# Performance work log

Hardware: AMD Instinct MI355X
Metric: run time of the kernel (lower is better)

## Reference

```python
import jax, jax.numpy as jnp
import numpy as np

B, T, E, M, V = 256, 256, 512, 16, 32000
EPS = 1e-6


def layer_norm(x, g, b):
    m = x.mean(-1, keepdims=True)
    v = x.var(-1, keepdims=True)
    return (x - m) / jnp.sqrt(v + EPS) * g + b


def setup_inputs() -> dict:
    key = jax.random.key(0)
    ks = jax.random.split(key, 12)
    s = 0.02
    return {
        "hidden_state": jax.random.normal(ks[0], (B, 1, E), jnp.float32),
        "output_sequence": jax.random.randint(ks[1], (B, T), 0, V),
        "emb_out": jax.random.normal(ks[2], (V, E), jnp.float32) * s,
        "Wq": jax.random.normal(ks[3], (E, E), jnp.float32) * s,
        "bq": jnp.zeros((E,), jnp.float32),
        "Wk": jax.random.normal(ks[4], (E, E), jnp.float32) * s,
        "bk": jnp.zeros((E,), jnp.float32),
        "Wv": jax.random.normal(ks[5], (E, E), jnp.float32) * s,
        "bv": jnp.zeros((E,), jnp.float32),
        "mover_w": jax.random.normal(ks[6], (M, E), jnp.float32) * s,  # decoder_mover.weight
        "gamma": jnp.ones((E,), jnp.float32),
        "beta": jnp.zeros((E,), jnp.float32),
        "vocab_W": jax.random.normal(ks[7], (E, V), jnp.float32) * s,
        "vocab_b": jnp.zeros((V,), jnp.float32),
    }


def reference(hidden_state, output_sequence, emb_out, Wq, bq, Wk, bk, Wv, bv,
              mover_w, gamma, beta, vocab_W, vocab_b):
    # Embeddings: lookup * sqrt(embed_dim) (annotated-transformer convention)
    x = emb_out[output_sequence] * jnp.sqrt(jnp.float32(E))  # [B, T, E]
    b = x.shape[0]
    # mover = (zeros_like(z)+1) * weight[None]  -> broadcast weight over batch
    mover = jnp.broadcast_to(mover_w[None], (b, M, E))
    # Precompute K/V projections of the constant mover rows once per step inside scan
    scale = 1.0 / jnp.sqrt(jnp.float32(E))

    def step(z, xt):                       # z: [B, E], xt: [B, E]
        z = z + xt
        g = jnp.concatenate([z[:, None, :], mover], axis=1)  # [B, 1+M, E]
        # only row 0 of dg is used -> query only the z token (same math)
        q = z @ Wq + bq                    # [B, E]
        k = g @ Wk + bk                    # [B, 1+M, E]
        v = g @ Wv + bv                    # [B, 1+M, E]
        att = jax.nn.softmax(jnp.einsum('be,bne->bn', q, k) * scale, axis=-1)
        dg0 = jnp.einsum('bn,bne->be', att, v)
        z = layer_norm(z + dg0, gamma, beta)
        return z, None

    z0 = hidden_state[:, 0, :]
    z, _ = jax.lax.scan(step, z0, jnp.swapaxes(x, 0, 1))
    z = z[:, None, :]                      # [B, 1, E]
    y = jax.nn.log_softmax(z @ vocab_W + vocab_b, axis=-1)  # [B, 1, V]
    return (z, y)
```

## Files before the change

### kernel.cpp

```cpp
#include <hip/hip_runtime.h>

#define B_ 256
#define T_ 256
#define E_ 512
#define V_ 32000
#define NMOV 16
#define NT 65
#define NCG 16
#define NBG 16
#define YSTR 1056
#define ZSTR 520

#define SQRTE 22.62741699796952f
#define SCALE 0.04419417382415922f

typedef __attribute__((ext_vector_type(8))) short bf16x8;
typedef __attribute__((ext_vector_type(4))) short bf16x4;
typedef __attribute__((ext_vector_type(4))) float f32x4;
typedef unsigned long long u64;

__device__ __forceinline__ short f2bf(float f) {
  unsigned u = __float_as_uint(f);
  u += 0x7fffu + ((u >> 16) & 1u);
  return (short)(u >> 16);
}
__device__ __forceinline__ float bf2f(short s) {
  return __uint_as_float(((unsigned)(unsigned short)s) << 16);
}

__device__ __forceinline__ float wredsum(float v) {
  int x;
  x = __builtin_amdgcn_update_dpp(0, __float_as_int(v), 0xB1, 0xF, 0xF, true);
  v += __int_as_float(x);
  x = __builtin_amdgcn_update_dpp(0, __float_as_int(v), 0x4E, 0xF, 0xF, true);
  v += __int_as_float(x);
  x = __builtin_amdgcn_update_dpp(0, __float_as_int(v), 0x141, 0xF, 0xF, true);
  v += __int_as_float(x);
  x = __builtin_amdgcn_update_dpp(0, __float_as_int(v), 0x140, 0xF, 0xF, true);
  v += __int_as_float(x);
  x = __builtin_amdgcn_update_dpp(0, __float_as_int(v), 0x142, 0xF, 0xF, true);
  v += __int_as_float(x);
  x = __builtin_amdgcn_update_dpp(0, __float_as_int(v), 0x143, 0xF, 0xF, true);
  v += __int_as_float(x);
  return __int_as_float(__builtin_amdgcn_readlane(__float_as_int(v), 63));
}

__device__ __forceinline__ bf16x8 aload8v(const short* p) {
  union { u64 u[2]; bf16x8 v; } c;
  c.u[0] = __hip_atomic_load((const u64*)p,       __ATOMIC_RELAXED, __HIP_MEMORY_SCOPE_AGENT);
  c.u[1] = __hip_atomic_load((const u64*)(p + 4), __ATOMIC_RELAXED, __HIP_MEMORY_SCOPE_AGENT);
  return c.v;
}
__device__ __forceinline__ void astore4v(short* p, bf16x4 v) {
  union { bf16x4 v; u64 u; } c; c.v = v;
  __hip_atomic_store((u64*)p, c.u, __ATOMIC_RELAXED, __HIP_MEMORY_SCOPE_AGENT);
}

__global__ void k_movers(const float* __restrict__ Wk, const float* __restrict__ bk,
                         const float* __restrict__ Wv, const float* __restrict__ bv,
                         const float* __restrict__ mover, float* __restrict__ kmvm)
{
  const int m = blockIdx.x & 15;
  const int s = blockIdx.x >> 4;
  const float* W  = s ? Wv : Wk;
  const float* bb = s ? bv : bk;
  const int c = threadIdx.x * 2;
  float a0 = bb[c], a1 = bb[c + 1];
  for (int r = 0; r < E_; ++r) {
    float mv = mover[m * E_ + r];
    float2 wv = *(const float2*)(W + (size_t)r * E_ + c);
    a0 += mv * wv.x; a1 += mv * wv.y;
  }
  kmvm[(s * NMOV + m) * E_ + c]     = a0;
  kmvm[(s * NMOV + m) * E_ + c + 1] = a1;
}

__global__ void k_gemmA(const float* __restrict__ Wq, const float* __restrict__ Wk,
                        float* __restrict__ A)
{
  const int ti = blockIdx.x >> 5, tj = blockIdx.x & 31;
  const int l = threadIdx.x, r16 = l & 15, kq = (l >> 4) * 8;
  f32x4 acc = {0.f, 0.f, 0.f, 0.f};
  for (int ks = 0; ks < 16; ++ks) {
    const float* ap = Wq + (size_t)(ti * 16 + r16) * E_ + ks * 32 + kq;
    const float* bp = Wk + (size_t)(tj * 16 + r16) * E_ + ks * 32 + kq;
    bf16x8 a, b;
    #pragma unroll
    for (int j = 0; j < 8; ++j) { a[j] = f2bf(ap[j]); b[j] = f2bf(bp[j]); }
    acc = __builtin_amdgcn_mfma_f32_16x16x32_bf16(a, b, acc, 0, 0, 0);
  }
  #pragma unroll
  for (int r = 0; r < 4; ++r)
    A[(size_t)(ti * 16 + (l >> 4) * 4 + r) * E_ + tj * 16 + r16] = acc[r];
}

__global__ void k_wqk(const float* __restrict__ Wq, const float* __restrict__ kmvm,
                      float* __restrict__ Wqk)
{
  const int i = blockIdx.x;
  const int l = threadIdx.x, m = l & 15, sl = l >> 4;
  float p = 0.f;
  for (int j = sl * 128; j < sl * 128 + 128; ++j)
    p += Wq[(size_t)i * E_ + j] * kmvm[(size_t)m * E_ + j];
  p += __shfl_xor(p, 16, 64);
  p += __shfl_xor(p, 32, 64);
  if (l < 16) Wqk[i * 16 + m] = p;
}

__global__ void k_cvec(const float* __restrict__ Wq, const float* __restrict__ Wk,
                       const float* __restrict__ bq, const float* __restrict__ bk,
                       float* __restrict__ cvec)
{
  const int i = blockIdx.x * 64 + threadIdx.x;
  float s = 0.f;
  for (int j = 0; j < E_; ++j)
    s += Wq[(size_t)i * E_ + j] * bk[j] + Wk[(size_t)i * E_ + j] * bq[j];
  cvec[i] = s;
}

__global__ void k_lb(const float* __restrict__ bq, const float* __restrict__ bk,
                     const float* __restrict__ kmvm, float* __restrict__ lb)
{
  const int l = threadIdx.x;
  if (l < 16) {
    float s = 0.f;
    for (int j = 0; j < E_; ++j) s += bq[j] * kmvm[(size_t)l * E_ + j];
    lb[l] = s;
  } else if (l == 16) {
    float s = 0.f;
    for (int j = 0; j < E_; ++j) s += bq[j] * bk[j];
    lb[16] = s;
  }
}

__global__ void k_pack(const float* __restrict__ A, const float* __restrict__ Wv,
                       const float* __restrict__ Wqk, short* __restrict__ Wfrag)
{
  const int blk = blockIdx.x;
  const int ct = blk >> 4, ks = blk & 15;
  const int l = threadIdx.x;
  const int c = ct * 16 + (l & 15);
  const int r0 = ks * 32 + (l >> 4) * 8;
  short v[8];
  #pragma unroll
  for (int j = 0; j < 8; ++j) {
    const int r = r0 + j;
    float x;
    if (c < 512)       x = A[(size_t)r * E_ + c];
    else if (c < 1024) x = Wv[(size_t)r * E_ + (c - 512)];
    else               x = Wqk[r * 16 + (c - 1024)];
    v[j] = f2bf(x);
  }
  *(bf16x8*)(Wfrag + ((size_t)blk * 64 + l) * 8) = *(const bf16x8*)v;
}

__global__ __launch_bounds__(512, 2) void k_scan5(
    const float* __restrict__ hidden, const int* __restrict__ seq,
    const float* __restrict__ emb,
    const float* __restrict__ gamma, const float* __restrict__ beta,
    const float* __restrict__ bv,
    const float* __restrict__ kmvm, const float* __restrict__ cvec,
    const float* __restrict__ lb, const short* __restrict__ Wfrag,
    short* __restrict__ Yx, unsigned* __restrict__ flags,
    float* __restrict__ zout)
{
  extern __shared__ char smem[];
  short* wlds = (short*)smem;
  short* zfs  = (short*)(smem + 81920);
  short* vml  = (short*)(smem + 98304);
  float* cl   = (float*)(smem + 114688);
  float* bvl  = (float*)(smem + 116736);
  float* gl   = (float*)(smem + 118784);
  float* bl   = (float*)(smem + 120832);
  float* lbl  = (float*)(smem + 122880);

  const int tid = threadIdx.x, l = tid & 63, w = tid >> 6;
  const int cg = blockIdx.x >> 4;
  const int bg = blockIdx.x & 15;
  const int ntiles = (cg == 15) ? 5 : 4;

  for (int i = tid; i < NMOV * E_; i += 512)
    vml[i] = f2bf(kmvm[NMOV * E_ + i]);
  for (int i = tid; i < E_; i += 512) {
    cl[i] = cvec[i]; bvl[i] = bv[i]; gl[i] = gamma[i]; bl[i] = beta[i];
  }
  if (tid < 17) lbl[tid] = lb[tid];
  {
    const bf16x8* src = (const bf16x8*)(Wfrag + (size_t)(cg * 4) * 16 * 64 * 8);
    bf16x8* dst = (bf16x8*)wlds;
    for (int i = tid; i < ntiles * 16 * 64; i += 512) dst[i] = src[i];
  }

  const int b0 = bg * 16 + w * 2;
  float zr[2][8];
  #pragma unroll
  for (int bi = 0; bi < 2; ++bi) {
    *(float4*)&zr[bi][0] = *(const float4*)(hidden + (size_t)(b0 + bi) * E_ + l * 8);
    *(float4*)&zr[bi][4] = *(const float4*)(hidden + (size_t)(b0 + bi) * E_ + l * 8 + 4);
  }

  const int sq0 = b0 * T_, sq1 = (b0 + 1) * T_;
  int ian = seq[sq0], ibn = seq[sq1];
  float4 ea0 = *(const float4*)(emb + (size_t)ian * E_ + l * 8);
  float4 ea1 = *(const float4*)(emb + (size_t)ian * E_ + l * 8 + 4);
  float4 eb0 = *(const float4*)(emb + (size_t)ibn * E_ + l * 8);
  float4 eb1 = *(const float4*)(emb + (size_t)ibn * E_ + l * 8 + 4);
  ian = seq[sq0 + 1]; ibn = seq[sq1 + 1];

  unsigned* const flagline = flags + bg * 32;
  __syncthreads();

  #pragma unroll 1
  for (int t = 0; t < T_; ++t) {
    const int p = t & 1;
    {
      float xa[8] = {ea0.x, ea0.y, ea0.z, ea0.w, ea1.x, ea1.y, ea1.z, ea1.w};
      float xb[8] = {eb0.x, eb0.y, eb0.z, eb0.w, eb1.x, eb1.y, eb1.z, eb1.w};
      short ta[8], tb[8];
      #pragma unroll
      for (int j = 0; j < 8; ++j) {
        zr[0][j] += xa[j] * SQRTE; ta[j] = f2bf(zr[0][j]);
        zr[1][j] += xb[j] * SQRTE; tb[j] = f2bf(zr[1][j]);
      }
      const int ks = l >> 2;
      const int ua = ((l & 3) << 4) | (w * 2);
      const int ub = ua | 1;
      *(bf16x8*)&zfs[((ks << 6) + (ua ^ (ks & 7))) * 8] = *(const bf16x8*)ta;
      *(bf16x8*)&zfs[((ks << 6) + (ub ^ (ks & 7))) * 8] = *(const bf16x8*)tb;
    }
    if (t + 1 < T_) {
      ea0 = *(const float4*)(emb + (size_t)ian * E_ + l * 8);
      ea1 = *(const float4*)(emb + (size_t)ian * E_ + l * 8 + 4);
      eb0 = *(const float4*)(emb + (size_t)ibn * E_ + l * 8);
      eb1 = *(const float4*)(emb + (size_t)ibn * E_ + l * 8 + 4);
      if (t + 2 < T_) { ian = seq[sq0 + t + 2]; ibn = seq[sq1 + t + 2]; }
    }
    __syncthreads();

    if (w < ntiles) {
      const int lt = w;
      f32x4 acc = {0.f, 0.f, 0.f, 0.f};
      #pragma unroll
      for (int ks = 0; ks < 16; ++ks) {
        bf16x8 wf = *(const bf16x8*)&wlds[((lt * 16 + ks) * 64 + l) * 8];
        bf16x8 zb = *(const bf16x8*)&zfs[((ks << 6) + (l ^ (ks & 7))) * 8];
        acc = __builtin_amdgcn_mfma_f32_16x16x32_bf16(wf, zb, acc, 0, 0, 0);
      }
      const int gt = cg * 4 + lt;
      bf16x4 o;
      #pragma unroll
      for (int r = 0; r < 4; ++r) o[r] = f2bf(acc[r]);
      astore4v(Yx + (((size_t)(p * NBG + bg) * 16) + (l & 15)) * YSTR
                  + gt * 16 + ((l >> 4) << 2), o);
      asm volatile("s_waitcnt vmcnt(0)" ::: "memory");
    }
    __syncthreads();

    if (tid == 0)
      __hip_atomic_store(&flagline[cg], (unsigned)(t + 1),
                         __ATOMIC_RELAXED, __HIP_MEMORY_SCOPE_AGENT);
    if (w == 0) {
      const unsigned rnd = (unsigned)(t + 1);
      const unsigned* fp = flagline + (l & 15);
      while (__hip_atomic_load(fp, __ATOMIC_RELAXED, __HIP_MEMORY_SCOPE_AGENT) < rnd)
        __builtin_amdgcn_s_sleep(1);
      asm volatile("" ::: "memory");
    }
    __syncthreads();

    {
      const short* Yb  = Yx + ((size_t)(p * NBG + bg) * 16) * YSTR;
      const short* Yr0 = Yb + (size_t)(w * 2) * YSTR;
      const short* Yr1 = Yb + (size_t)(w * 2 + 1) * YSTR;
      bf16x8 wv0 = aload8v(Yr0 + l * 8),       wv1 = aload8v(Yr1 + l * 8);
      bf16x8 vv0 = aload8v(Yr0 + 512 + l * 8), vv1 = aload8v(Yr1 + 512 + l * 8);
      bf16x8 ma0 = aload8v(Yr0 + 1024),        ma1 = aload8v(Yr1 + 1024);
      bf16x8 mb0 = aload8v(Yr0 + 1032),        mb1 = aload8v(Yr1 + 1032);

      float cw[8];
      *(float4*)&cw[0] = *(const float4*)&cl[l * 8];
      *(float4*)&cw[4] = *(const float4*)&cl[l * 8 + 4];
      float p0 = 0.f, p1 = 0.f;
      #pragma unroll
      for (int j = 0; j < 8; ++j) {
        p0 += (bf2f(wv0[j]) + cw[j]) * zr[0][j];
        p1 += (bf2f(wv1[j]) + cw[j]) * zr[1][j];
      }
      const float r0 = wredsum(p0);
      const float r1 = wredsum(p1);

      float a0[17], a1[17];
      a0[0] = (r0 + lbl[16]) * SCALE;
      a1[0] = (r1 + lbl[16]) * SCALE;
      #pragma unroll
      for (int m = 0; m < 8; ++m) {
        a0[m + 1] = (bf2f(ma0[m]) + lbl[m]) * SCALE;
        a0[m + 9] = (bf2f(mb0[m]) + lbl[m + 8]) * SCALE;
        a1[m + 1] = (bf2f(ma1[m]) + lbl[m]) * SCALE;
        a1[m + 9] = (bf2f(mb1[m]) + lbl[m + 8]) * SCALE;
      }
      float mx0 = a0[0], mx1 = a1[0];
      #pragma unroll
      for (int n = 1; n < 17; ++n) { mx0 = fmaxf(mx0, a0[n]); mx1 = fmaxf(mx1, a1[n]); }
      float d0 = 0.f, d1 = 0.f;
      #pragma unroll
      for (int n = 0; n < 17; ++n) {
        a0[n] = __expf(a0[n] - mx0); d0 += a0[n];
        a1[n] = __expf(a1[n] - mx1); d1 += a1[n];
      }
      const float rd0 = __fdividef(1.f, d0);
      const float rd1 = __fdividef(1.f, d1);

      float bw[8];
      *(float4*)&bw[0] = *(const float4*)&bvl[l * 8];
      *(float4*)&bw[4] = *(const float4*)&bvl[l * 8 + 4];
      float u0[8], u1[8];
      #pragma unroll
      for (int j = 0; j < 8; ++j) {
        u0[j] = a0[0] * (bf2f(vv0[j]) + bw[j]);
        u1[j] = a1[0] * (bf2f(vv1[j]) + bw[j]);
      }
      #pragma unroll
      for (int m = 0; m < 16; ++m) {
        const bf16x8 vm = *(const bf16x8*)&vml[m * E_ + l * 8];
        #pragma unroll
        for (int j = 0; j < 8; ++j) {
          const float f = bf2f(vm[j]);
          u0[j] += a0[m + 1] * f;
          u1[j] += a1[m + 1] * f;
        }
      }
      #pragma unroll
      for (int j = 0; j < 8; ++j) {
        u0[j] = zr[0][j] + u0[j] * rd0;
        u1[j] = zr[1][j] + u1[j] * rd1;
      }

      float s10 = 0.f, s20 = 0.f, s11 = 0.f, s21 = 0.f;
      #pragma unroll
      for (int j = 0; j < 8; ++j) {
        s10 += u0[j]; s20 += u0[j] * u0[j];
        s11 += u1[j]; s21 += u1[j] * u1[j];
      }
      s10 = wredsum(s10); s20 = wredsum(s20);
      s11 = wredsum(s11); s21 = wredsum(s21);
      const float mean0 = s10 * (1.f / 512.f);
      const float mean1 = s11 * (1.f / 512.f);
      const float rstd0 = rsqrtf(s20 * (1.f / 512.f) - mean0 * mean0 + 1e-6f);
      const float rstd1 = rsqrtf(s21 * (1.f / 512.f) - mean1 * mean1 + 1e-6f);

      float gw[8], bb[8];
      *(float4*)&gw[0] = *(const float4*)&gl[l * 8];
      *(float4*)&gw[4] = *(const float4*)&gl[l * 8 + 4];
      *(float4*)&bb[0] = *(const float4*)&bl[l * 8];
      *(float4*)&bb[4] = *(const float4*)&bl[l * 8 + 4];
      #pragma unroll
      for (int j = 0; j < 8; ++j) {
        zr[0][j] = (u0[j] - mean0) * rstd0 * gw[j] + bb[j];
        zr[1][j] = (u1[j] - mean1) * rstd1 * gw[j] + bb[j];
      }
    }
  }

  if (cg == 0) {
    #pragma unroll
    for (int bi = 0; bi < 2; ++bi) {
      *(float4*)(zout + (size_t)(b0 + bi) * E_ + l * 8)     = *(float4*)&zr[bi][0];
      *(float4*)(zout + (size_t)(b0 + bi) * E_ + l * 8 + 4) = *(float4*)&zr[bi][4];
    }
  }
}

#define K2_SMEM (128 * ZSTR * 2)

__global__ __launch_bounds__(512, 2) void k_logits(
    const float* __restrict__ z, const float* __restrict__ W,
    const float* __restrict__ bia, float* __restrict__ out)
{
  extern __shared__ short zl[];
  const int tid = threadIdx.x;
  const int btile = blockIdx.x & 1;
  const int vt = blockIdx.x >> 1;
  for (int i = tid; i < 128 * 128; i += 512) {
    int row = i >> 7, c4 = (i & 127) << 2;
    float4 zv = *(const float4*)(z + (size_t)(btile * 128 + row) * E_ + c4);
    short* d = zl + row * ZSTR + c4;
    d[0] = f2bf(zv.x); d[1] = f2bf(zv.y); d[2] = f2bf(zv.z); d[3] = f2bf(zv.w);
  }
  __syncthreads();
  const int lane = tid & 63, w = tid >> 6;
  const int vc = vt * 128 + w * 16 + (lane & 15);
  const int kq = (lane >> 4) * 8;
  f32x4 acc[8];
  #pragma unroll
  for (int rt = 0; rt < 8; ++rt) acc[rt] = (f32x4){0.f, 0.f, 0.f, 0.f};
  for (int ks = 0; ks < 16; ++ks) {
    bf16x8 bf;
    #pragma unroll
    for (int j = 0; j < 8; ++j)
      bf[j] = f2bf(W[(size_t)(ks * 32 + kq + j) * V_ + vc]);
    #pragma unroll
    for (int rt = 0; rt < 8; ++rt) {
      bf16x8 a = *(const bf16x8*)&zl[(rt * 16 + (lane & 15)) * ZSTR + ks * 32 + kq];
      acc[rt] = __builtin_amdgcn_mfma_f32_16x16x32_bf16(a, bf, acc[rt], 0, 0, 0);
    }
  }
  const float bbv = bia[vc];
  #pragma unroll
  for (int rt = 0; rt < 8; ++rt)
    #pragma unroll
    for (int r = 0; r < 4; ++r)
      out[(size_t)(btile * 128 + rt * 16 + (lane >> 4) * 4 + r) * V_ + vc] = acc[rt][r] + bbv;
}

__global__ void k_logsoftmax(float* __restrict__ y)
{
  float* L = y + (size_t)blockIdx.x * V_;
  float m = -3.402823466e+38f, s = 0.f;
  for (int i = threadIdx.x; i < V_; i += 256) {
    float l = L[i];
    if (l > m) { s = s * __expf(m - l) + 1.f; m = l; }
    else       { s += __expf(l - m); }
  }
  #pragma unroll
  for (int k = 1; k < 64; k <<= 1) {
    float m2 = __shfl_xor(m, k, 64);
    float s2 = __shfl_xor(s, k, 64);
    float M = fmaxf(m, m2);
    s = s * __expf(m - M) + s2 * __expf(m2 - M);
    m = M;
  }
  __shared__ float ms[4], ss[4];
  if ((threadIdx.x & 63) == 0) { ms[threadIdx.x >> 6] = m; ss[threadIdx.x >> 6] = s; }
  __syncthreads();
  float M = fmaxf(fmaxf(ms[0], ms[1]), fmaxf(ms[2], ms[3]));
  float S = ss[0] * __expf(ms[0] - M) + ss[1] * __expf(ms[1] - M) +
            ss[2] * __expf(ms[2] - M) + ss[3] * __expf(ms[3] - M);
  const float lse = M + logf(S);
  for (int i = threadIdx.x; i < V_; i += 256) L[i] -= lse;
}

#define SCAN_SMEM 123008

extern "C" void kernel_launch(void* const* d_in, const int* in_sizes, int n_in,
                              void* d_out, int out_size, void* d_ws, size_t ws_size,
                              hipStream_t stream) {
  const float* hidden = (const float*)d_in[0];
  const int*   seq    = (const int*)  d_in[1];
  const float* emb    = (const float*)d_in[2];
  const float* Wq     = (const float*)d_in[3];
  const float* bq     = (const float*)d_in[4];
  const float* Wk     = (const float*)d_in[5];
  const float* bk     = (const float*)d_in[6];
  const float* Wv     = (const float*)d_in[7];
  const float* bv     = (const float*)d_in[8];
  const float* mover  = (const float*)d_in[9];
  const float* gamma  = (const float*)d_in[10];
  const float* beta   = (const float*)d_in[11];
  const float* vocabW = (const float*)d_in[12];
  const float* vocabB = (const float*)d_in[13];

  float* zoutp = (float*)d_out;
  float* yout  = zoutp + (size_t)B_ * E_;

  short*    Wfrag = (short*)yout;
  float*    A     = yout + 266240;
  float*    Wqk   = A + 262144;
  float*    cvec  = Wqk + 8192;
  float*    lbp   = cvec + 512;
  float*    kmvmS = lbp + 32;
  short*    Yx    = (short*)(kmvmS + 16384);
  unsigned* flags = (unsigned*)(Yx + 540672);

  hipMemsetAsync(flags, 0, 16 * 32 * 4, stream);
  hipLaunchKernelGGL(k_movers, dim3(32), dim3(256), 0, stream, Wk, bk, Wv, bv, mover, kmvmS);
  hipLaunchKernelGGL(k_gemmA,  dim3(1024), dim3(64), 0, stream, Wq, Wk, A);
  hipLaunchKernelGGL(k_wqk,    dim3(512), dim3(64), 0, stream, Wq, kmvmS, Wqk);
  hipLaunchKernelGGL(k_cvec,   dim3(8), dim3(64), 0, stream, Wq, Wk, bq, bk, cvec);
  hipLaunchKernelGGL(k_lb,     dim3(1), dim3(64), 0, stream, bq, bk, kmvmS, lbp);
  hipLaunchKernelGGL(k_pack,   dim3(NT * 16), dim3(64), 0, stream, A, Wv, Wqk, Wfrag);

  hipFuncSetAttribute((const void*)k_scan5, hipFuncAttributeMaxDynamicSharedMemorySize, SCAN_SMEM);
  void* args[] = {(void*)&hidden, (void*)&seq, (void*)&emb,
                  (void*)&gamma, (void*)&beta, (void*)&bv,
                  (void*)&kmvmS, (void*)&cvec, (void*)&lbp, (void*)&Wfrag,
                  (void*)&Yx, (void*)&flags, (void*)&zoutp};
  hipLaunchCooperativeKernel((const void*)k_scan5, dim3(NCG * NBG), dim3(512),
                             args, SCAN_SMEM, stream);

  hipFuncSetAttribute((const void*)k_logits, hipFuncAttributeMaxDynamicSharedMemorySize, K2_SMEM);
  hipLaunchKernelGGL(k_logits, dim3(500), dim3(512), K2_SMEM, stream, zoutp, vocabW, vocabB, yout);
  hipLaunchKernelGGL(k_logsoftmax, dim3(256), dim3(256), 0, stream, yout);
}
```

Baseline: 1.521 ms.

## Compute mover attention-weighted sum with MFMA and wave-parallel softmax

```diff
diff --git a/kernel.cpp b/kernel.cpp
--- a/kernel.cpp
+++ b/kernel.cpp
@@ -43,6 +43,33 @@
   x = __builtin_amdgcn_update_dpp(0, __float_as_int(v), 0x143, 0xF, 0xF, true);
   v += __int_as_float(x);
   return __int_as_float(__builtin_amdgcn_readlane(__float_as_int(v), 63));
+}
+__device__ __forceinline__ float rowmax16(float v) {
+  int x;
+  x = __builtin_amdgcn_update_dpp(0, __float_as_int(v), 0xB1, 0xF, 0xF, true);
+  v = fmaxf(v, __int_as_float(x));
+  x = __builtin_amdgcn_update_dpp(0, __float_as_int(v), 0x4E, 0xF, 0xF, true);
+  v = fmaxf(v, __int_as_float(x));
+  x = __builtin_amdgcn_update_dpp(0, __float_as_int(v), 0x141, 0xF, 0xF, true);
+  v = fmaxf(v, __int_as_float(x));
+  x = __builtin_amdgcn_update_dpp(0, __float_as_int(v), 0x140, 0xF, 0xF, true);
+  v = fmaxf(v, __int_as_float(x));
+  return v;
+}
+__device__ __forceinline__ float rowsum16(float v) {
+  int x;
+  x = __builtin_amdgcn_update_dpp(0, __float_as_int(v), 0xB1, 0xF, 0xF, true);
+  v += __int_as_float(x);
+  x = __builtin_amdgcn_update_dpp(0, __float_as_int(v), 0x4E, 0xF, 0xF, true);
+  v += __int_as_float(x);
+  x = __builtin_amdgcn_update_dpp(0, __float_as_int(v), 0x141, 0xF, 0xF, true);
+  v += __int_as_float(x);
+  x = __builtin_amdgcn_update_dpp(0, __float_as_int(v), 0x140, 0xF, 0xF, true);
+  v += __int_as_float(x);
+  return v;
+}
+__device__ __forceinline__ float rdlane(float v, int lane) {
+  return __int_as_float(__builtin_amdgcn_readlane(__float_as_int(v), lane));
 }
 
 __device__ __forceinline__ bf16x8 aload8v(const short* p) {
@@ -154,7 +181,7 @@
   *(bf16x8*)(Wfrag + ((size_t)blk * 64 + l) * 8) = *(const bf16x8*)v;
 }
 
-__global__ __launch_bounds__(512, 2) void k_scan5(
+__global__ __launch_bounds__(512, 2) void k_scan6(
     const float* __restrict__ hidden, const int* __restrict__ seq,
     const float* __restrict__ emb,
     const float* __restrict__ gamma, const float* __restrict__ beta,
@@ -165,31 +192,45 @@
     float* __restrict__ zout)
 {
   extern __shared__ char smem[];
-  short* wlds = (short*)smem;
-  short* zfs  = (short*)(smem + 81920);
-  short* vml  = (short*)(smem + 98304);
-  float* cl   = (float*)(smem + 114688);
-  float* bvl  = (float*)(smem + 116736);
-  float* gl   = (float*)(smem + 118784);
-  float* bl   = (float*)(smem + 120832);
-  float* lbl  = (float*)(smem + 122880);
+  short* wlds    = (short*)smem;
+  short* zfs     = (short*)(smem + 81920);
+  short* vmfragT = (short*)(smem + 98304);
+  float* umov    = (float*)(smem + 114688);
+  short* attf    = (short*)(smem + 147968);
 
   const int tid = threadIdx.x, l = tid & 63, w = tid >> 6;
   const int cg = blockIdx.x >> 4;
   const int bg = blockIdx.x & 15;
   const int ntiles = (cg == 15) ? 5 : 4;
-
-  for (int i = tid; i < NMOV * E_; i += 512)
-    vml[i] = f2bf(kmvm[NMOV * E_ + i]);
-  for (int i = tid; i < E_; i += 512) {
-    cl[i] = cvec[i]; bvl[i] = bv[i]; gl[i] = gamma[i]; bl[i] = beta[i];
-  }
-  if (tid < 17) lbl[tid] = lb[tid];
+  const int lm = l & 15;
+
+  for (int i = tid; i < 32 * 32; i += 512) {
+    const int tile = i >> 5, ln = i & 31;
+    const int m0 = (ln >> 4) * 8, c = tile * 16 + (ln & 15);
+    short tmp[8];
+    #pragma unroll
+    for (int j = 0; j < 8; ++j)
+      tmp[j] = f2bf(kmvm[NMOV * E_ + (size_t)(m0 + j) * E_ + c]);
+    *(bf16x8*)&vmfragT[((size_t)tile * 32 + ln) * 8] = *(const bf16x8*)tmp;
+  }
+  for (int i = tid; i < 16 * 40; i += 512) attf[i] = 0;
   {
     const bf16x8* src = (const bf16x8*)(Wfrag + (size_t)(cg * 4) * 16 * 64 * 8);
     bf16x8* dst = (bf16x8*)wlds;
     for (int i = tid; i < ntiles * 16 * 64; i += 512) dst[i] = src[i];
   }
+
+  float cw[8], bw[8], gw[8], bb[8];
+  *(float4*)&cw[0] = *(const float4*)(cvec  + l * 8);
+  *(float4*)&cw[4] = *(const float4*)(cvec  + l * 8 + 4);
+  *(float4*)&bw[0] = *(const float4*)(bv    + l * 8);
+  *(float4*)&bw[4] = *(const float4*)(bv    + l * 8 + 4);
+  *(float4*)&gw[0] = *(const float4*)(gamma + l * 8);
+  *(float4*)&gw[4] = *(const float4*)(gamma + l * 8 + 4);
+  *(float4*)&bb[0] = *(const float4*)(beta  + l * 8);
+  *(float4*)&bb[4] = *(const float4*)(beta  + l * 8 + 4);
+  const float lbw  = lb[lm];
+  const float lb16 = lb[16];
 
   const int b0 = bg * 16 + w * 2;
   float zr[2][8];
@@ -238,19 +279,18 @@
     __syncthreads();
 
     if (w < ntiles) {
-      const int lt = w;
       f32x4 acc = {0.f, 0.f, 0.f, 0.f};
       #pragma unroll
       for (int ks = 0; ks < 16; ++ks) {
-        bf16x8 wf = *(const bf16x8*)&wlds[((lt * 16 + ks) * 64 + l) * 8];
+        bf16x8 wf = *(const bf16x8*)&wlds[((w * 16 + ks) * 64 + l) * 8];
         bf16x8 zb = *(const bf16x8*)&zfs[((ks << 6) + (l ^ (ks & 7))) * 8];
         acc = __builtin_amdgcn_mfma_f32_16x16x32_bf16(wf, zb, acc, 0, 0, 0);
       }
-      const int gt = cg * 4 + lt;
+      const int gt = cg * 4 + w;
       bf16x4 o;
       #pragma unroll
       for (int r = 0; r < 4; ++r) o[r] = f2bf(acc[r]);
-      astore4v(Yx + (((size_t)(p * NBG + bg) * 16) + (l & 15)) * YSTR
+      astore4v(Yx + (((size_t)(p * NBG + bg) * 16) + lm) * YSTR
                   + gt * 16 + ((l >> 4) << 2), o);
       asm volatile("s_waitcnt vmcnt(0)" ::: "memory");
     }
@@ -259,83 +299,73 @@
     if (tid == 0)
       __hip_atomic_store(&flagline[cg], (unsigned)(t + 1),
                          __ATOMIC_RELAXED, __HIP_MEMORY_SCOPE_AGENT);
-    if (w == 0) {
+    {
       const unsigned rnd = (unsigned)(t + 1);
-      const unsigned* fp = flagline + (l & 15);
-      while (__hip_atomic_load(fp, __ATOMIC_RELAXED, __HIP_MEMORY_SCOPE_AGENT) < rnd)
+      for (;;) {
+        unsigned f = __hip_atomic_load(&flagline[lm], __ATOMIC_RELAXED,
+                                       __HIP_MEMORY_SCOPE_AGENT);
+        if (__all(lm == cg || f >= rnd)) break;
         __builtin_amdgcn_s_sleep(1);
+      }
       asm volatile("" ::: "memory");
     }
+
+    const short* Yb  = Yx + ((size_t)(p * NBG + bg) * 16) * YSTR;
+    const short* Yr0 = Yb + (size_t)(w * 2) * YSTR;
+    const short* Yr1 = Yb + (size_t)(w * 2 + 1) * YSTR;
+    bf16x8 wv0 = aload8v(Yr0 + l * 8),       wv1 = aload8v(Yr1 + l * 8);
+    bf16x8 vv0 = aload8v(Yr0 + 512 + l * 8), vv1 = aload8v(Yr1 + 512 + l * 8);
+    const short* Yrh = (l < 32) ? Yr0 : Yr1;
+    short mlr = (short)__hip_atomic_load((const short*)(Yrh + 1024 + lm),
+                                         __ATOMIC_RELAXED, __HIP_MEMORY_SCOPE_AGENT);
+
+    float p0 = 0.f, p1 = 0.f;
+    #pragma unroll
+    for (int j = 0; j < 8; ++j) {
+      p0 += (bf2f(wv0[j]) + cw[j]) * zr[0][j];
+      p1 += (bf2f(wv1[j]) + cw[j]) * zr[1][j];
+    }
+    const float dl0 = (wredsum(p0) + lb16) * SCALE;
+    const float dl1 = (wredsum(p1) + lb16) * SCALE;
+
+    const float dl   = (l < 32) ? dl0 : dl1;
+    const float lgt  = (bf2f(mlr) + lbw) * SCALE;
+    const float mx   = fmaxf(rowmax16(lgt), dl);
+    const float e    = __expf(lgt - mx);
+    const float a0v  = __expf(dl - mx);
+    const float den  = rowsum16(e) + a0v;
+    if ((l & 16) == 0)
+      attf[(w * 2 + (l >> 5)) * 40 + lm] = f2bf(e);
+
+    const float a00 = rdlane(a0v, 0),  a01 = rdlane(a0v, 32);
+    const float rd0 = __fdividef(1.f, rdlane(den, 0));
+    const float rd1 = __fdividef(1.f, rdlane(den, 32));
+
     __syncthreads();
 
+    #pragma unroll
+    for (int tt = 0; tt < 4; ++tt) {
+      const int tile = w * 4 + tt;
+      bf16x8 af = {0, 0, 0, 0, 0, 0, 0, 0};
+      if (l < 32) af = *(const bf16x8*)&vmfragT[((size_t)tile * 32 + l) * 8];
+      bf16x8 bf = *(const bf16x8*)&attf[lm * 40 + (l >> 4) * 8];
+      f32x4 z4 = {0.f, 0.f, 0.f, 0.f};
+      z4 = __builtin_amdgcn_mfma_f32_16x16x32_bf16(af, bf, z4, 0, 0, 0);
+      *(f32x4*)&umov[(size_t)lm * 520 + tile * 16 + ((l >> 4) << 2)] = z4;
+    }
+    __syncthreads();
+
     {
-      const short* Yb  = Yx + ((size_t)(p * NBG + bg) * 16) * YSTR;
-      const short* Yr0 = Yb + (size_t)(w * 2) * YSTR;
-      const short* Yr1 = Yb + (size_t)(w * 2 + 1) * YSTR;
-      bf16x8 wv0 = aload8v(Yr0 + l * 8),       wv1 = aload8v(Yr1 + l * 8);
-      bf16x8 vv0 = aload8v(Yr0 + 512 + l * 8), vv1 = aload8v(Yr1 + 512 + l * 8);
-      bf16x8 ma0 = aload8v(Yr0 + 1024),        ma1 = aload8v(Yr1 + 1024);
-      bf16x8 mb0 = aload8v(Yr0 + 1032),        mb1 = aload8v(Yr1 + 1032);
-
-      float cw[8];
-      *(float4*)&cw[0] = *(const float4*)&cl[l * 8];
-      *(float4*)&cw[4] = *(const float4*)&cl[l * 8 + 4];
-      float p0 = 0.f, p1 = 0.f;
+      float um0[8], um1[8], u0[8], u1[8];
+      *(float4*)&um0[0] = *(const float4*)&umov[(size_t)(w * 2) * 520 + l * 8];
+      *(float4*)&um0[4] = *(const float4*)&umov[(size_t)(w * 2) * 520 + l * 8 + 4];
+      *(float4*)&um1[0] = *(const float4*)&umov[(size_t)(w * 2 + 1) * 520 + l * 8];
+      *(float4*)&um1[4] = *(const float4*)&umov[(size_t)(w * 2 + 1) * 520 + l * 8 + 4];
       #pragma unroll
       for (int j = 0; j < 8; ++j) {
-        p0 += (bf2f(wv0[j]) + cw[j]) * zr[0][j];
-        p1 += (bf2f(wv1[j]) + cw[j]) * zr[1][j];
+        u0[j] = zr[0][j] + (a00 * (bf2f(vv0[j]) + bw[j]) + um0[j]) * rd0;
+        u1[j] = zr[1][j] + (a01 * (bf2f(vv1[j]) + bw[j]) + um1[j]) * rd1;
       }
-      const float r0 = wredsum(p0);
-      const float r1 = wredsum(p1);
-
-      float a0[17], a1[17];
-      a0[0] = (r0 + lbl[16]) * SCALE;
-      a1[0] = (r1 + lbl[16]) * SCALE;
-      #pragma unroll
-      for (int m = 0; m < 8; ++m) {
-        a0[m + 1] = (bf2f(ma0[m]) + lbl[m]) * SCALE;
-        a0[m + 9] = (bf2f(mb0[m]) + lbl[m + 8]) * SCALE;
-        a1[m + 1] = (bf2f(ma1[m]) + lbl[m]) * SCALE;
-        a1[m + 9] = (bf2f(mb1[m]) + lbl[m + 8]) * SCALE;
-      }
-      float mx0 = a0[0], mx1 = a1[0];
-      #pragma unroll
-      for (int n = 1; n < 17; ++n) { mx0 = fmaxf(mx0, a0[n]); mx1 = fmaxf(mx1, a1[n]); }
-      float d0 = 0.f, d1 = 0.f;
-      #pragma unroll
-      for (int n = 0; n < 17; ++n) {
-        a0[n] = __expf(a0[n] - mx0); d0 += a0[n];
-        a1[n] = __expf(a1[n] - mx1); d1 += a1[n];
-      }
-      const float rd0 = __fdividef(1.f, d0);
-      const float rd1 = __fdividef(1.f, d1);
-
-      float bw[8];
-      *(float4*)&bw[0] = *(const float4*)&bvl[l * 8];
-      *(float4*)&bw[4] = *(const float4*)&bvl[l * 8 + 4];
-      float u0[8], u1[8];
-      #pragma unroll
-      for (int j = 0; j < 8; ++j) {
-        u0[j] = a0[0] * (bf2f(vv0[j]) + bw[j]);
-        u1[j] = a1[0] * (bf2f(vv1[j]) + bw[j]);
-      }
-      #pragma unroll
-      for (int m = 0; m < 16; ++m) {
-        const bf16x8 vm = *(const bf16x8*)&vml[m * E_ + l * 8];
-        #pragma unroll
-        for (int j = 0; j < 8; ++j) {
-          const float f = bf2f(vm[j]);
-          u0[j] += a0[m + 1] * f;
-          u1[j] += a1[m + 1] * f;
-        }
-      }
-      #pragma unroll
-      for (int j = 0; j < 8; ++j) {
-        u0[j] = zr[0][j] + u0[j] * rd0;
-        u1[j] = zr[1][j] + u1[j] * rd1;
-      }
-
       float s10 = 0.f, s20 = 0.f, s11 = 0.f, s21 = 0.f;
       #pragma unroll
       for (int j = 0; j < 8; ++j) {
@@ -348,12 +378,6 @@
       const float mean1 = s11 * (1.f / 512.f);
       const float rstd0 = rsqrtf(s20 * (1.f / 512.f) - mean0 * mean0 + 1e-6f);
       const float rstd1 = rsqrtf(s21 * (1.f / 512.f) - mean1 * mean1 + 1e-6f);
-
-      float gw[8], bb[8];
-      *(float4*)&gw[0] = *(const float4*)&gl[l * 8];
-      *(float4*)&gw[4] = *(const float4*)&gl[l * 8 + 4];
-      *(float4*)&bb[0] = *(const float4*)&bl[l * 8];
-      *(float4*)&bb[4] = *(const float4*)&bl[l * 8 + 4];
       #pragma unroll
       for (int j = 0; j < 8; ++j) {
         zr[0][j] = (u0[j] - mean0) * rstd0 * gw[j] + bb[j];
@@ -440,7 +464,7 @@
   for (int i = threadIdx.x; i < V_; i += 256) L[i] -= lse;
 }
 
-#define SCAN_SMEM 123008
+#define SCAN_SMEM 149248
 
 extern "C" void kernel_launch(void* const* d_in, const int* in_sizes, int n_in,
                               void* d_out, int out_size, void* d_ws, size_t ws_size,
@@ -480,12 +504,12 @@
   hipLaunchKernelGGL(k_lb,     dim3(1), dim3(64), 0, stream, bq, bk, kmvmS, lbp);
   hipLaunchKernelGGL(k_pack,   dim3(NT * 16), dim3(64), 0, stream, A, Wv, Wqk, Wfrag);
 
-  hipFuncSetAttribute((const void*)k_scan5, hipFuncAttributeMaxDynamicSharedMemorySize, SCAN_SMEM);
+  hipFuncSetAttribute((const void*)k_scan6, hipFuncAttributeMaxDynamicSharedMemorySize, SCAN_SMEM);
   void* args[] = {(void*)&hidden, (void*)&seq, (void*)&emb,
                   (void*)&gamma, (void*)&beta, (void*)&bv,
                   (void*)&kmvmS, (void*)&cvec, (void*)&lbp, (void*)&Wfrag,
                   (void*)&Yx, (void*)&flags, (void*)&zoutp};
-  hipLaunchCooperativeKernel((const void*)k_scan5, dim3(NCG * NBG), dim3(512),
+  hipLaunchCooperativeKernel((const void*)k_scan6, dim3(NCG * NBG), dim3(512),
                              args, SCAN_SMEM, stream);
 
   hipFuncSetAttribute((const void*)k_logits, hipFuncAttributeMaxDynamicSharedMemorySize, K2_SMEM);
```

Result: faster. 1.298 ms (-14.7%).
